# Kernel tuning notes

Measured on AMD Instinct MI355X. Metric: run time of the kernel, lower is better.

Reference implementation:

```python
import jax, jax.numpy as jnp
import numpy as np

B, N, D, H, HID = 8, 729, 1152, 12, 4304
HD = D // H
EPS = 1e-6


def _layer_norm(x, g, b):
    mu = jnp.mean(x, axis=-1, keepdims=True)
    var = jnp.mean((x - mu) ** 2, axis=-1, keepdims=True)
    return (x - mu) / jnp.sqrt(var + EPS) * g + b


def setup_inputs() -> dict:
    key = jax.random.key(0)
    ks = jax.random.split(key, 9)
    s = 0.02
    return {
        "x": jax.random.normal(ks[0], (B, N, D), jnp.float32),
        "wq": jax.random.normal(ks[1], (D, D), jnp.float32) * s,
        "bq": jnp.zeros((D,), jnp.float32),
        "wk": jax.random.normal(ks[2], (D, D), jnp.float32) * s,
        "bk": jnp.zeros((D,), jnp.float32),
        "wv": jax.random.normal(ks[3], (D, D), jnp.float32) * s,
        "bv": jnp.zeros((D,), jnp.float32),
        "wo": jax.random.normal(ks[4], (D, D), jnp.float32) * s,
        "bo": jnp.zeros((D,), jnp.float32),
        "ln1_g": jnp.ones((D,), jnp.float32),
        "ln1_b": jnp.zeros((D,), jnp.float32),
        "w_fc1": jax.random.normal(ks[5], (HID, D), jnp.float32) * s,
        "b_fc1": jnp.zeros((HID,), jnp.float32),
        "w_fc2": jax.random.normal(ks[6], (D, HID), jnp.float32) * s,
        "b_fc2": jnp.zeros((D,), jnp.float32),
        "ln2_g": jnp.ones((D,), jnp.float32),
        "ln2_b": jnp.zeros((D,), jnp.float32),
    }


def reference(x, wq, bq, wk, bk, wv, bv, wo, bo, ln1_g, ln1_b,
              w_fc1, b_fc1, w_fc2, b_fc2, ln2_g, ln2_b):
    b, n, d = x.shape
    # split_heads in the source is a plain view (B, H, N, HD) -- NOT a transpose.
    def heads(t):
        return t.reshape(b, H, n, HD)

    Q = heads(x @ wq.T + bq)
    K = heads(x @ wk.T + bk)
    V = heads(x @ wv.T + bv)

    scores = jnp.einsum("bhqd,bhkd->bhqk", Q, K) * (HD ** -0.5)
    attn_w = jax.nn.softmax(scores, axis=-1)
    o = jnp.einsum("bhqk,bhkd->bhqd", attn_w, V)  # [B,H,N,HD]
    o = jnp.swapaxes(o, 1, 2).reshape(b, n, d)
    attn_out = o @ wo.T + bo

    # post-norm: LN(sublayer) + residual
    h = _layer_norm(attn_out, ln1_g, ln1_b) + x

    # quirky MLP: activation applied BEFORE fc1 (faithful to source)
    m = jax.nn.gelu(h, approximate=True)
    m = m @ w_fc1.T + b_fc1
    m = m @ w_fc2.T + b_fc2

    return _layer_norm(m, ln2_g, ln2_b) + h
```

## Files before the change

### kernel.cpp

```cpp
#include <hip/hip_runtime.h>
#include <hip/hip_bf16.h>

#define BF16 __hip_bfloat16

typedef short short8 __attribute__((ext_vector_type(8)));
typedef short short4v __attribute__((ext_vector_type(4)));
typedef float v4f __attribute__((ext_vector_type(4)));
typedef float f4 __attribute__((ext_vector_type(4)));

__device__ float g_bp[1152];
__device__ BF16  g_wm[1152 * 1152];

__device__ __forceinline__ short f2bs(float f) {
    __hip_bfloat16 h = __float2bfloat16(f);
    return *(short*)&h;
}

__device__ __forceinline__ float bs2f(short s) {
    __hip_bfloat16 h = *(__hip_bfloat16*)&s;
    return __bfloat162float(h);
}

__device__ __forceinline__ void async_cp16(const BF16* g, BF16* l) {
    __builtin_amdgcn_global_load_lds(
        (const __attribute__((address_space(1))) void*)g,
        (__attribute__((address_space(3))) void*)l,
        16, 0, 0);
}

__device__ __forceinline__ int xcd_chunk(int u, int nwg) {
    int xcd = u & 7, i = u >> 3;
    int q = nwg >> 3, r = nwg & 7;
    return (xcd < r ? xcd * (q + 1) : r * (q + 1) + (xcd - r) * q) + i;
}

__global__ __launch_bounds__(256) void prep_kernel(
    const float* __restrict__ wq, const float* __restrict__ wk,
    const float* __restrict__ wv, const float* __restrict__ wo,
    const float* __restrict__ wfc1, const float* __restrict__ wfc2,
    const float* __restrict__ x,
    const float* __restrict__ bfc1, const float* __restrict__ bfc2,
    BF16* __restrict__ wbq, BF16* __restrict__ wbk,
    BF16* __restrict__ wbv, BF16* __restrict__ wbo,
    BF16* __restrict__ wbf1t, BF16* __restrict__ wbf2,
    BF16* __restrict__ xb)
{
    __shared__ float tile[64][65];
    const int bid = blockIdx.x;
    const int tid = threadIdx.x;

    if (bid < 16641) {
        const int i = bid * 256 + tid;
        constexpr int N_DD  = 331776;
        constexpr int N4    = 4 * N_DD;
        constexpr int N_F2  = 1253376;
        constexpr int E_F2  = N4 + N_F2;
        constexpr int N_X   = 1679616;
        constexpr int TOTAL = E_F2 + N_X;

        if (i < N4) {
            int seg = i / N_DD, j = i - seg * N_DD;
            const float* s = (seg == 0) ? wq : (seg == 1) ? wk : (seg == 2) ? wv : wo;
            BF16* d = (seg == 0) ? wbq : (seg == 1) ? wbk : (seg == 2) ? wbv : wbo;
            f4 v = ((const f4*)s)[j];
            short4v o = {f2bs(v.x), f2bs(v.y), f2bs(v.z), f2bs(v.w)};
            ((short4v*)d)[j] = o;
        } else if (i < E_F2) {
            int j = i - N4;
            int row = j / 1088;
            int c = (j - row * 1088) * 4;
            short4v o = {0, 0, 0, 0};
            if (c < 4304) {
                f4 v = *(const f4*)(wfc2 + (size_t)row * 4304 + c);
                o[0] = f2bs(v.x); o[1] = f2bs(v.y); o[2] = f2bs(v.z); o[3] = f2bs(v.w);
            }
            *(short4v*)(wbf2 + (size_t)row * 4352 + c) = o;
        } else if (i < TOTAL) {
            int j = i - E_F2;
            f4 v = ((const f4*)x)[j];
            short4v o = {f2bs(v.x), f2bs(v.y), f2bs(v.z), f2bs(v.w)};
            ((short4v*)xb)[j] = o;
        }
    } else if (bid < 17865) {
        const int b2 = bid - 16641;
        const int h0 = (b2 % 68) * 64;
        const int d0 = (b2 / 68) * 64;
#pragma unroll
        for (int i = 0; i < 4; ++i) {
            int lin = tid + i * 256;
            int r = lin >> 4, c4 = lin & 15;
            f4 v = {0.f, 0.f, 0.f, 0.f};
            if (h0 + r < 4304)
                v = *(const f4*)(wfc1 + (size_t)(h0 + r) * 1152 + d0 + c4 * 4);
            tile[r][c4 * 4 + 0] = v.x;
            tile[r][c4 * 4 + 1] = v.y;
            tile[r][c4 * 4 + 2] = v.z;
            tile[r][c4 * 4 + 3] = v.w;
        }
        __syncthreads();
#pragma unroll
        for (int i = 0; i < 2; ++i) {
            int lin = tid + i * 256;
            int dr = lin >> 3, h8 = lin & 7;
            short8 o;
#pragma unroll
            for (int e = 0; e < 8; ++e)
                o[e] = f2bs(tile[h8 * 8 + e][dr]);
            *(short8*)(wbf1t + (size_t)(d0 + dr) * 4352 + h0 + h8 * 8) = o;
        }
    } else {
        const int row = (bid - 17865) * 4 + (tid >> 6);
        const int lane = tid & 63;
        const float* wr = wfc2 + (size_t)row * 4304;
        float s = 0.f;
        for (int k = lane; k < 4304; k += 64) s += wr[k] * bfc1[k];
#pragma unroll
        for (int mm = 1; mm < 64; mm <<= 1) s += __shfl_xor(s, mm, 64);
        if (lane == 0) g_bp[row] = s + bfc2[row];
    }
}

__global__ __launch_bounds__(512, 2) void qkv_wm8_kernel(
    const BF16* __restrict__ A,
    const BF16* __restrict__ Wqkv,
    const float* __restrict__ b0, const float* __restrict__ b1,
    const float* __restrict__ b2,
    BF16* __restrict__ C, size_t cstride, int M,
    const BF16* __restrict__ W2,
    const BF16* __restrict__ W1t)
{
    __shared__ __align__(16) BF16 smem[65536];
    const int bid  = blockIdx.x;
    const int tid  = threadIdx.x;
    const int lane = tid & 63;
    const int wave = tid >> 6;
    const int quad = lane >> 4;
    const int l16  = lane & 15;
    const v4f zf = {0.f, 0.f, 0.f, 0.f};

    int rr[2], sw[2], lo[2];
#pragma unroll
    for (int j = 0; j < 2; ++j) {
        int c = tid + j * 512;
        rr[j] = c >> 3;
        sw[j] = (((c & 7) - (c >> 3)) & 7) << 3;
        lo[j] = (c & ~63) * 8;
    }

    if (bid < 81) {
        BF16* Am = smem;
        BF16* Bm = smem + 8192;
        const int m0 = (bid % 9) * 128;
        const int n0 = (bid / 9) * 128;
        const int wm = (wave >> 1) * 32;
        const int wn = (wave & 1) * 64;

        v4f acc[2][4];
#pragma unroll
        for (int i = 0; i < 2; ++i)
#pragma unroll
            for (int j = 0; j < 4; ++j) acc[i][j] = zf;

        const BF16* gA[2]; const BF16* gB[2];
#pragma unroll
        for (int j = 0; j < 2; ++j) {
            gA[j] = W2 + (size_t)(m0 + rr[j]) * 4352 + sw[j];
            gB[j] = W1t + (size_t)(n0 + rr[j]) * 4352 + sw[j];
        }

        for (int kt = 0; kt < 68; ++kt) {
#pragma unroll
            for (int j = 0; j < 2; ++j) { async_cp16(gA[j], Am + lo[j]); gA[j] += 64; }
#pragma unroll
            for (int j = 0; j < 2; ++j) { async_cp16(gB[j], Bm + lo[j]); gB[j] += 64; }
            __syncthreads();
#pragma unroll
            for (int ks = 0; ks < 2; ++ks) {
                short8 af[2], bfg[4];
#pragma unroll
                for (int mt = 0; mt < 2; ++mt) {
                    int row = wm + mt * 16 + l16;
                    af[mt] = *(const short8*)(Am + row * 64 + ((((ks << 2) | quad) + row & 7) & 7) * 8);
                }
#pragma unroll
                for (int nt = 0; nt < 4; ++nt) {
                    int row = wn + nt * 16 + l16;
                    bfg[nt] = *(const short8*)(Bm + row * 64 + ((((ks << 2) | quad) + row & 7) & 7) * 8);
                }
#pragma unroll
                for (int mt = 0; mt < 2; ++mt)
#pragma unroll
                    for (int nt = 0; nt < 4; ++nt)
                        acc[mt][nt] = __builtin_amdgcn_mfma_f32_16x16x32_bf16(
                            af[mt], bfg[nt], acc[mt][nt], 0, 0, 0);
            }
            __syncthreads();
        }

#pragma unroll
        for (int mt = 0; mt < 2; ++mt)
#pragma unroll
            for (int nt = 0; nt < 4; ++nt)
#pragma unroll
                for (int r2 = 0; r2 < 4; ++r2) {
                    int row_l = wm + mt * 16 + quad * 4 + r2;
                    int col_l = wn + nt * 16 + l16;
                    smem[row_l * 128 + col_l] = __float2bfloat16(acc[mt][nt][r2]);
                }
        __syncthreads();
#pragma unroll
        for (int p = 0; p < 4; ++p) {
            int idx = p * 512 + tid;
            *(short8*)(g_wm + (size_t)(m0 + (idx >> 4)) * 1152 + n0 + (idx & 15) * 8) =
                *(const short8*)(smem + idx * 8);
        }
    } else {
        const int wg = xcd_chunk(bid - 81, 322);
        const int m0 = (wg / 14) * 256;
        const int n0 = (wg % 14) * 256;
        const int wr = wave >> 2;
        const int wc = wave & 3;
        BF16* As = smem;
        BF16* Bs = smem + 32768;

        v4f acc[8][4];
#pragma unroll
        for (int i = 0; i < 8; ++i)
#pragma unroll
            for (int j = 0; j < 4; ++j) acc[i][j] = zf;

        #define STAGE_A(dd, hh, tt)                                            \
            {                                                                  \
                _Pragma("unroll")                                              \
                for (int j = 0; j < 2; ++j)                                    \
                    async_cp16(A + (size_t)(m0 + (hh) * 128 + rr[j]) * 1152    \
                                 + (tt) * 64 + sw[j],                          \
                               As + (dd) * 16384 + (hh) * 8192 + lo[j]);       \
            }
        #define STAGE_B(dd, hh, tt)                                            \
            {                                                                  \
                _Pragma("unroll")                                              \
                for (int j = 0; j < 2; ++j)                                    \
                    async_cp16(Wqkv + (size_t)(n0 + (hh) * 128 + rr[j]) * 1152 \
                                 + (tt) * 64 + sw[j],                          \
                               Bs + (dd) * 16384 + (hh) * 8192 + lo[j]);       \
            }

        STAGE_B(0, 0, 0); STAGE_B(0, 1, 0);
        STAGE_A(0, 0, 0); STAGE_A(0, 1, 0);
        STAGE_B(1, 0, 1); STAGE_B(1, 1, 1);
        asm volatile("s_waitcnt vmcnt(4)" ::: "memory");
        __builtin_amdgcn_s_barrier();
        __builtin_amdgcn_sched_barrier(0);

        short8 bfr[4][2], afr[2][2];
#pragma unroll 2
        for (int it = 0; it < 18; ++it) {
            const int d = it & 1;
            const BF16* Ad = As + d * 16384;
            const BF16* Bd = Bs + d * 16384;
#pragma unroll
            for (int q = 0; q < 4; ++q) {
                if (q == 0) {
#pragma unroll
                    for (int nt = 0; nt < 4; ++nt) {
                        int R = wc * 64 + nt * 16 + l16;
#pragma unroll
                        for (int ks = 0; ks < 2; ++ks)
                            bfr[nt][ks] = *(const short8*)(
                                Bd + R * 64 + ((((ks << 2) | quad) + R & 7) & 7) * 8);
                    }
                }
#pragma unroll
                for (int mi = 0; mi < 2; ++mi) {
                    int R = wr * 128 + (q * 2 + mi) * 16 + l16;
#pragma unroll
                    for (int ks = 0; ks < 2; ++ks)
                        afr[mi][ks] = *(const short8*)(
                            Ad + R * 64 + ((((ks << 2) | quad) + R & 7) & 7) * 8);
                }
                if (q == 0) { if (it + 1 < 18) STAGE_A(d ^ 1, 0, it + 1); }
                if (q == 1) { if (it + 1 < 18) STAGE_A(d ^ 1, 1, it + 1); }
                if (q == 2) { if (it + 2 < 18) STAGE_B(d,     0, it + 2); }
                if (q == 3) { if (it + 2 < 18) STAGE_B(d,     1, it + 2); }

                __builtin_amdgcn_s_barrier();
                asm volatile("s_waitcnt lgkmcnt(0)" ::: "memory");
                __builtin_amdgcn_sched_barrier(0);
                __builtin_amdgcn_s_setprio(1);
#pragma unroll
                for (int ks = 0; ks < 2; ++ks)
#pragma unroll
                    for (int mi = 0; mi < 2; ++mi)
#pragma unroll
                        for (int nt = 0; nt < 4; ++nt)
                            acc[q * 2 + mi][nt] = __builtin_amdgcn_mfma_f32_16x16x32_bf16(
                                afr[mi][ks], bfr[nt][ks], acc[q * 2 + mi][nt], 0, 0, 0);
                __builtin_amdgcn_s_setprio(0);
                if (q == 3) {
                    if (it + 2 < 18)
                        asm volatile("s_waitcnt vmcnt(4)" ::: "memory");
                    else
                        asm volatile("s_waitcnt vmcnt(0)" ::: "memory");
                }
                __builtin_amdgcn_s_barrier();
            }
        }
        #undef STAGE_A
        #undef STAGE_B

        float bv[4];
        int csel[4];
#pragma unroll
        for (int nt = 0; nt < 4; ++nt) {
            int col_g = n0 + wc * 64 + nt * 16 + l16;
            int sel = (col_g >= 2304) ? 2 : (col_g >= 1152) ? 1 : 0;
            csel[nt] = sel;
            const float* bp = (sel == 0) ? b0 : (sel == 1) ? b1 : b2;
            bv[nt] = (col_g < 3456) ? bp[col_g - sel * 1152] : 0.f;
        }
#pragma unroll
        for (int mt = 0; mt < 8; ++mt)
#pragma unroll
            for (int nt = 0; nt < 4; ++nt)
#pragma unroll
                for (int r2 = 0; r2 < 4; ++r2) {
                    int row_l = wr * 128 + mt * 16 + quad * 4 + r2;
                    int col_l = wc * 64 + nt * 16 + l16;
                    smem[row_l * 256 + col_l] = __float2bfloat16(acc[mt][nt][r2] + bv[nt]);
                }
        (void)csel;
        __syncthreads();
#pragma unroll
        for (int p = 0; p < 16; ++p) {
            int idx = p * 512 + tid;
            int row = m0 + (idx >> 5);
            int col_g = n0 + (idx & 31) * 8;
            if (row < M && col_g < 3456) {
                int sel = (col_g >= 2304) ? 2 : (col_g >= 1152) ? 1 : 0;
                *(short8*)(C + (size_t)sel * cstride + (size_t)row * 1152
                           + col_g - sel * 1152) =
                    *(const short8*)(smem + idx * 8);
            }
        }
    }
}

__global__ __launch_bounds__(256) void trans_kernel(
    const BF16* __restrict__ V, BF16* __restrict__ VT)
{
    __shared__ __align__(16) BF16 tl[64][128];
    const int bid = blockIdx.x, tid = threadIdx.x;
    const short8 zero8 = {0, 0, 0, 0, 0, 0, 0, 0};

    if (bid < 1152) {
        const int hg = bid / 12, kb = bid - hg * 12;
        const int b = hg / 12, hh = hg - b * 12;
        const BF16* src = V + (size_t)b * 839808 + (size_t)hh * 69984;
        BF16* dst = VT + (size_t)hg * 86016;
        const int kk0 = kb * 64;
#pragma unroll
        for (int i = 0; i < 3; ++i) {
            int c = tid + i * 256;
            int r = c / 12, cg = c - r * 12;
            short8 v = (kk0 + r < 729)
                ? *(const short8*)(src + (size_t)(kk0 + r) * 96 + cg * 8) : zero8;
            *(short8*)(&tl[r][(cg ^ ((r >> 3) & 7)) * 8]) = v;
        }
        __syncthreads();
#pragma unroll
        for (int i = 0; i < 3; ++i) {
            int wc = tid + i * 256;
            int hd = wc >> 3, o = wc & 7;
            int sp = (((hd >> 3) ^ o) << 3) + (hd & 7);
            short8 out;
#pragma unroll
            for (int j = 0; j < 8; ++j)
                out[j] = *(const short*)&tl[o * 8 + j][sp];
            *(short8*)(dst + (size_t)hd * 768 + kk0 + o * 8) = out;
        }
    } else {
        int c = (bid - 1152) * 256 + tid;
        int hg = c / 1536, rem = c - hg * 1536;
        int r = rem / 96, ock = rem - r * 96;
        int kk = ock * 8;
        short8 v = zero8;
        if (r == 0) {
            const short oneb = 0x3F80;
#pragma unroll
            for (int j = 0; j < 8; ++j) v[j] = (kk + j < 729) ? oneb : (short)0;
        }
        *(short8*)(VT + (size_t)hg * 86016 + (size_t)(96 + r) * 768 + kk) = v;
    }
}

template<int TM>
__global__ __launch_bounds__(256) void gemm_bt_t(
    const BF16* __restrict__ A, int lda,
    const BF16* __restrict__ W, int ldb,
    const float* __restrict__ bias, int nbias,
    BF16* __restrict__ C, int ldc,
    int M, int Kr, int nbn)
{
    constexpr int MT = TM / 32;
    __shared__ __align__(16) BF16 smem[(TM + 128) * 64];
    BF16* As = smem;
    BF16* Bs = smem + TM * 64;

    const int tid  = threadIdx.x;
    const int lane = tid & 63;
    const int wave = tid >> 6;
    const int quad = lane >> 4;
    const int l16  = lane & 15;
    const int wm   = (wave >> 1) * (TM / 2);
    const int wn   = (wave & 1) * 64;
    const int wg   = xcd_chunk(blockIdx.x, gridDim.x);
    const int m0   = (wg / nbn) * TM;
    const int n0   = (wg % nbn) * 128;
    if (m0 >= M) return;

    const v4f zf = {0.f, 0.f, 0.f, 0.f};
    v4f acc[MT][4];
#pragma unroll
    for (int i = 0; i < MT; ++i)
#pragma unroll
        for (int j = 0; j < 4; ++j) acc[i][j] = zf;

    const BF16* gA[MT]; BF16* lA[MT];
#pragma unroll
    for (int i = 0; i < MT; ++i) {
        int c = tid + i * 256;
        gA[i] = A + (size_t)(m0 + (c >> 3)) * lda + ((((c & 7) - (c >> 3)) & 7) << 3);
        lA[i] = As + (c & ~63) * 8;
    }
    const BF16* gB[4]; BF16* lB[4];
#pragma unroll
    for (int i = 0; i < 4; ++i) {
        int c = tid + i * 256;
        gB[i] = W + (size_t)(n0 + (c >> 3)) * ldb + ((((c & 7) - (c >> 3)) & 7) << 3);
        lB[i] = Bs + (c & ~63) * 8;
    }

    const int nk = Kr >> 6;
    for (int kt = 0; kt < nk; ++kt) {
#pragma unroll
        for (int i = 0; i < MT; ++i) { async_cp16(gA[i], lA[i]); gA[i] += 64; }
#pragma unroll
        for (int i = 0; i < 4; ++i)  { async_cp16(gB[i], lB[i]); gB[i] += 64; }
        __syncthreads();

#pragma unroll
        for (int ks = 0; ks < 2; ++ks) {
            short8 af[MT], bfg[4];
#pragma unroll
            for (int mt = 0; mt < MT; ++mt) {
                int row = wm + mt * 16 + l16;
                af[mt] = *(const short8*)(As + row * 64 + ((((ks << 2) | quad) + row & 7) & 7) * 8);
            }
#pragma unroll
            for (int nt = 0; nt < 4; ++nt) {
                int row = wn + nt * 16 + l16;
                bfg[nt] = *(const short8*)(Bs + row * 64 + ((((ks << 2) | quad) + row & 7) & 7) * 8);
            }
#pragma unroll
            for (int mt = 0; mt < MT; ++mt)
#pragma unroll
                for (int nt = 0; nt < 4; ++nt)
                    acc[mt][nt] = __builtin_amdgcn_mfma_f32_16x16x32_bf16(
                        af[mt], bfg[nt], acc[mt][nt], 0, 0, 0);
        }
        __syncthreads();
    }

    float bv[4];
#pragma unroll
    for (int nt = 0; nt < 4; ++nt) {
        int col = n0 + wn + nt * 16 + l16;
        bv[nt] = (col < nbias) ? bias[col] : 0.f;
    }
#pragma unroll
    for (int mt = 0; mt < MT; ++mt)
#pragma unroll
        for (int nt = 0; nt < 4; ++nt)
#pragma unroll
            for (int r2 = 0; r2 < 4; ++r2) {
                int row_l = wm + mt * 16 + quad * 4 + r2;
                int col_l = wn + nt * 16 + l16;
                smem[row_l * 128 + col_l] = __float2bfloat16(acc[mt][nt][r2] + bv[nt]);
            }
    __syncthreads();
#pragma unroll
    for (int p = 0; p < TM / 16; ++p) {
        int idx = p * 256 + tid;
        int row = m0 + (idx >> 4);
        if (row < M)
            *(short8*)(C + (size_t)row * ldc + n0 + (idx & 15) * 8) =
                *(const short8*)(smem + idx * 8);
    }
}

__global__ __launch_bounds__(256) void attn_flash3(
    const BF16* __restrict__ Q, const BF16* __restrict__ K,
    const BF16* __restrict__ VT, BF16* __restrict__ O)
{
    constexpr int NQ = 729, HDk = 96, DM = 1152, LDV = 768;
    __shared__ __align__(16) BF16 Ks[64 * 104];
    __shared__ __align__(16) BF16 Vs[112 * 64];
    __shared__ __align__(16) BF16 Ps[4][32 * 64];

    const int id = blockIdx.x;
    const int xcd = id & 7, slot = id >> 3;
    const int hb = slot / 6, qt = slot - hb * 6;
    const int hg = xcd * 12 + hb;
    const int b = hg / 12, hh = hg - b * 12;

    const int tid = threadIdx.x, wave = tid >> 6, lane = tid & 63;
    const int quad = lane >> 4, l16 = lane & 15;
    const size_t kbase = (size_t)b * (NQ * DM) + (size_t)hh * (NQ * HDk);
    const size_t vbase = (size_t)hg * 112 * LDV;

    const short8 zero8 = {0, 0, 0, 0, 0, 0, 0, 0};
    const v4f zf = {0.f, 0.f, 0.f, 0.f};
    const float C2 = 0.14724445f;

    const int q0w = qt * 128 + wave * 32;
    short8 aq[2][3];
#pragma unroll
    for (int mt = 0; mt < 2; ++mt) {
        int qrow = q0w + mt * 16 + l16;
#pragma unroll
        for (int ks = 0; ks < 3; ++ks)
            aq[mt][ks] = (qrow < NQ)
                ? *(const short8*)(Q + kbase + (size_t)qrow * HDk + ks * 32 + quad * 8)
                : zero8;
    }

    int kk_[3], kg_[3];
#pragma unroll
    for (int i = 0; i < 3; ++i) {
        int c = tid + i * 256;
        kk_[i] = c / 12; kg_[i] = c - kk_[i] * 12;
    }
    int vq_[4], vgr_[4], vhd_[4];
#pragma unroll
    for (int i = 0; i < 4; ++i) {
        int q = wave + 4 * i;
        vq_[i] = q;
        int hd = q * 8 + (lane >> 3);
        vhd_[i] = hd;
        vgr_[i] = ((lane & 7) - hd) & 7;
    }

    v4f oacc[2][7];
#pragma unroll
    for (int mt = 0; mt < 2; ++mt)
#pragma unroll
        for (int nt = 0; nt < 7; ++nt) oacc[mt][nt] = zf;

    short8 kreg[3];
#pragma unroll
    for (int i = 0; i < 3; ++i)
        kreg[i] = *(const short8*)(K + kbase + (size_t)kk_[i] * HDk + kg_[i] * 8);

    for (int kt = 0; kt < 12; ++kt) {
        const int k0 = kt * 64;
#pragma unroll
        for (int i = 0; i < 3; ++i)
            *(short8*)(Ks + kk_[i] * 104 + kg_[i] * 8) = kreg[i];
#pragma unroll
        for (int i = 0; i < 4; ++i) {
            if (vq_[i] < 14)
                async_cp16(VT + vbase + (size_t)vhd_[i] * LDV + k0 + vgr_[i] * 8,
                           Vs + vq_[i] * 512);
        }
        asm volatile("s_waitcnt lgkmcnt(0)" ::: "memory");
        __builtin_amdgcn_s_barrier();
        __builtin_amdgcn_sched_barrier(0);
        {
            const int kn = (kt < 11) ? (k0 + 64) : 0;
#pragma unroll
            for (int i = 0; i < 3; ++i)
                kreg[i] = *(const short8*)(K + kbase + (size_t)(kn + kk_[i]) * HDk + kg_[i] * 8);
        }

        v4f s[2][4];
#pragma unroll
        for (int mt = 0; mt < 2; ++mt)
#pragma unroll
            for (int nt = 0; nt < 4; ++nt) s[mt][nt] = zf;
#pragma unroll
        for (int ks = 0; ks < 3; ++ks)
#pragma unroll
            for (int nt = 0; nt < 4; ++nt) {
                short8 bk = *(const short8*)(Ks + (nt * 16 + l16) * 104 + ks * 32 + quad * 8);
#pragma unroll
                for (int mt = 0; mt < 2; ++mt)
                    s[mt][nt] = __builtin_amdgcn_mfma_f32_16x16x32_bf16(
                        aq[mt][ks], bk, s[mt][nt], 0, 0, 0);
            }

        BF16* Pw = &Ps[wave][0];
#pragma unroll
        for (int mt = 0; mt < 2; ++mt)
#pragma unroll
            for (int nt = 0; nt < 4; ++nt)
#pragma unroll
                for (int r = 0; r < 4; ++r)
                    Pw[((mt * 16 + quad * 4 + r) << 6)
                       + ((((nt << 1) | (l16 >> 3)) ^ (quad << 1)) << 3)
                       + (l16 & 7)] =
                        __float2bfloat16(exp2f(s[mt][nt][r] * C2));
        asm volatile("s_waitcnt lgkmcnt(0)" ::: "memory");

        short8 ap[2][2];
#pragma unroll
        for (int mt = 0; mt < 2; ++mt)
#pragma unroll
            for (int kc = 0; kc < 2; ++kc)
                ap[mt][kc] = *(const short8*)(Pw + ((mt * 16 + l16) << 6)
                    + ((((kc << 2) | quad) ^ (((l16 >> 2) & 3) << 1)) << 3));

        asm volatile("s_waitcnt vmcnt(3)" ::: "memory");
        __builtin_amdgcn_s_barrier();
        __builtin_amdgcn_sched_barrier(0);

#pragma unroll
        for (int nt = 0; nt < 7; ++nt) {
            int hd = nt * 16 + l16;
#pragma unroll
            for (int kc = 0; kc < 2; ++kc) {
                short8 bv = *(const short8*)(Vs + hd * 64 + (((kc * 4 + quad) + hd & 7) & 7) * 8);
#pragma unroll
                for (int mt = 0; mt < 2; ++mt)
                    oacc[mt][nt] = __builtin_amdgcn_mfma_f32_16x16x32_bf16(
                        ap[mt][kc], bv, oacc[mt][nt], 0, 0, 0);
            }
        }
        asm volatile("s_waitcnt lgkmcnt(0)" ::: "memory");
        __builtin_amdgcn_s_barrier();
        __builtin_amdgcn_sched_barrier(0);
    }

#pragma unroll
    for (int mt = 0; mt < 2; ++mt) {
        const int qb = q0w + mt * 16 + quad * 4;
#pragma unroll
        for (int r = 0; r < 4; ++r) {
            int q = qb + r;
            float lv = __shfl(oacc[mt][6][r], quad << 4, 64);
            float inv = (lv > 0.f) ? 1.f / lv : 0.f;
            if (q >= NQ) continue;
#pragma unroll
            for (int nt = 0; nt < 6; ++nt)
                O[(size_t)b * (NQ * DM) + (size_t)q * DM + hh * HDk + nt * 16 + l16] =
                    __float2bfloat16(oacc[mt][nt][r] * inv);
        }
    }
}

__device__ __forceinline__ float block_sum256(float v, float* red, int tid)
{
#pragma unroll
    for (int mm = 1; mm < 64; mm <<= 1) v += __shfl_xor(v, mm, 64);
    if ((tid & 63) == 0) red[tid >> 6] = v;
    __syncthreads();
    float r = red[0] + red[1] + red[2] + red[3];
    __syncthreads();
    return r;
}

__global__ __launch_bounds__(256) void ln1_gelu_kernel(
    const BF16* __restrict__ ao, const float* __restrict__ x,
    const float* __restrict__ gw, const float* __restrict__ bw,
    BF16* __restrict__ hout, BF16* __restrict__ gout)
{
    __shared__ float red[4];
    const int row = blockIdx.x, tid = threadIdx.x;
    const bool act = tid < 144;
    float v[8];
    float s = 0.f;
    if (act) {
        short8 pk = ((const short8*)(ao + (size_t)row * 1152))[tid];
#pragma unroll
        for (int j = 0; j < 8; ++j) { v[j] = bs2f(pk[j]); s += v[j]; }
    } else {
#pragma unroll
        for (int j = 0; j < 8; ++j) v[j] = 0.f;
    }
    s = block_sum256(s, red, tid);
    float mu = s * (1.f / 1152.f);
    float vsum = 0.f;
    if (act) {
#pragma unroll
        for (int j = 0; j < 8; ++j) { float d = v[j] - mu; vsum += d * d; }
    }
    vsum = block_sum256(vsum, red, tid);
    float rstd = rsqrtf(vsum * (1.f / 1152.f) + 1e-6f);
    if (act) {
        f4 g0 = ((const f4*)gw)[2 * tid], g1 = ((const f4*)gw)[2 * tid + 1];
        f4 b0 = ((const f4*)bw)[2 * tid], b1 = ((const f4*)bw)[2 * tid + 1];
        const f4* xr = (const f4*)(x + (size_t)row * 1152);
        f4 x0 = xr[2 * tid], x1 = xr[2 * tid + 1];
        short8 ho, go;
#pragma unroll
        for (int j = 0; j < 8; ++j) {
            float gj = (j < 4) ? g0[j] : g1[j - 4];
            float bj = (j < 4) ? b0[j] : b1[j - 4];
            float xj = (j < 4) ? x0[j] : x1[j - 4];
            float hv = (v[j] - mu) * rstd * gj + bj + xj;
            ho[j] = f2bs(hv);
            float t = hv;
            float gl = 0.5f * t * (1.f + tanhf(0.7978845608028654f * (t + 0.044715f * t * t * t)));
            go[j] = f2bs(gl);
        }
        ((short8*)(hout + (size_t)row * 1152))[tid] = ho;
        ((short8*)(gout + (size_t)row * 1152))[tid] = go;
    }
}

__global__ __launch_bounds__(256) void ln2_kernel(
    const BF16* __restrict__ m2, const BF16* __restrict__ hf,
    const float* __restrict__ gw, const float* __restrict__ bw,
    float* __restrict__ out)
{
    __shared__ float red[4];
    const int row = blockIdx.x, tid = threadIdx.x;
    const bool act = tid < 144;
    float v[8];
    float s = 0.f;
    if (act) {
        short8 pk = ((const short8*)(m2 + (size_t)row * 1152))[tid];
#pragma unroll
        for (int j = 0; j < 8; ++j) { v[j] = bs2f(pk[j]); s += v[j]; }
    } else {
#pragma unroll
        for (int j = 0; j < 8; ++j) v[j] = 0.f;
    }
    s = block_sum256(s, red, tid);
    float mu = s * (1.f / 1152.f);
    float vsum = 0.f;
    if (act) {
#pragma unroll
        for (int j = 0; j < 8; ++j) { float d = v[j] - mu; vsum += d * d; }
    }
    vsum = block_sum256(vsum, red, tid);
    float rstd = rsqrtf(vsum * (1.f / 1152.f) + 1e-6f);
    if (act) {
        f4 g0 = ((const f4*)gw)[2 * tid], g1 = ((const f4*)gw)[2 * tid + 1];
        f4 b0 = ((const f4*)bw)[2 * tid], b1 = ((const f4*)bw)[2 * tid + 1];
        short8 hfv = ((const short8*)(hf + (size_t)row * 1152))[tid];
        f4 o0, o1;
#pragma unroll
        for (int j = 0; j < 8; ++j) {
            float gj = (j < 4) ? g0[j] : g1[j - 4];
            float bj = (j < 4) ? b0[j] : b1[j - 4];
            float ov = (v[j] - mu) * rstd * gj + bj + bs2f(hfv[j]);
            if (j < 4) o0[j] = ov; else o1[j - 4] = ov;
        }
        f4* orow = (f4*)(out + (size_t)row * 1152);
        orow[2 * tid] = o0;
        orow[2 * tid + 1] = o1;
    }
}

extern "C" void kernel_launch(void* const* d_in, const int* in_sizes, int n_in,
                              void* d_out, int out_size, void* d_ws, size_t ws_size,
                              hipStream_t stream)
{
    const float* x    = (const float*)d_in[0];
    const float* wq   = (const float*)d_in[1];
    const float* bq   = (const float*)d_in[2];
    const float* wk   = (const float*)d_in[3];
    const float* bk   = (const float*)d_in[4];
    const float* wv   = (const float*)d_in[5];
    const float* bv   = (const float*)d_in[6];
    const float* wo   = (const float*)d_in[7];
    const float* bo   = (const float*)d_in[8];
    const float* ln1g = (const float*)d_in[9];
    const float* ln1b = (const float*)d_in[10];
    const float* wfc1 = (const float*)d_in[11];
    const float* bfc1 = (const float*)d_in[12];
    const float* wfc2 = (const float*)d_in[13];
    const float* bfc2 = (const float*)d_in[14];
    const float* ln2g = (const float*)d_in[15];
    const float* ln2b = (const float*)d_in[16];

    const int T = 8 * 729;
    const int D = 1152, HIDP = 4352;
    const size_t TD = (size_t)T * D;
    const size_t WDD = (size_t)D * D;

    BF16* wbq   = (BF16*)d_ws;
    BF16* wbk   = wbq + WDD;
    BF16* wbv   = wbk + WDD;
    BF16* wbo   = wbv + WDD;
    BF16* wbf1t = wbo + WDD;
    BF16* wbf2  = wbf1t + (size_t)HIDP * D;
    BF16* xb    = wbf2 + (size_t)D * HIDP;
    BF16* S0    = xb + TD;
    BF16* S1    = S0 + TD;
    BF16* S2    = S1 + TD;
    BF16* S3    = S2 + TD;
    BF16* C0    = S3 + TD;
    BF16* C1    = C0 + TD;
    BF16* VT    = C0;

    static float* bp_dev = nullptr;
    static BF16*  wm_dev = nullptr;
    if (!bp_dev) hipGetSymbolAddress((void**)&bp_dev, HIP_SYMBOL(g_bp));
    if (!wm_dev) hipGetSymbolAddress((void**)&wm_dev, HIP_SYMBOL(g_wm));

    dim3 blk(256);

    prep_kernel<<<18153, blk, 0, stream>>>(
        wq, wk, wv, wo, wfc1, wfc2, x, bfc1, bfc2,
        wbq, wbk, wbv, wbo, wbf1t, wbf2, xb);

    qkv_wm8_kernel<<<403, dim3(512), 0, stream>>>(
        xb, wbq, bq, bk, bv, S0, TD, T, wbf2, wbf1t);

    trans_kernel<<<1728, blk, 0, stream>>>(S2, VT);

    attn_flash3<<<576, blk, 0, stream>>>(S0, S1, VT, S3);

    gemm_bt_t<64><<<828, blk, 0, stream>>>(S3, D, wbo, D, bo, D, C0, D, T, D, 9);

    ln1_gelu_kernel<<<T, blk, 0, stream>>>(C0, x, ln1g, ln1b, C1, C0);

    gemm_bt_t<64><<<828, blk, 0, stream>>>(C0, D, wm_dev, D, bp_dev, D, S3, D, T, D, 9);

    ln2_kernel<<<T, blk, 0, stream>>>(S3, C1, ln2g, ln2b, (float*)d_out);
}
```

Measured before the change: 384.6 us.

## Read K directly from global in attention, shrink LN blocks, use exp-based GELU

New measurement: 408.9 us. 1.06x slower.

```diff
diff --git a/kernel.cpp b/kernel.cpp
--- a/kernel.cpp
+++ b/kernel.cpp
@@ -310,12 +310,10 @@
         #undef STAGE_B
 
         float bv[4];
-        int csel[4];
 #pragma unroll
         for (int nt = 0; nt < 4; ++nt) {
             int col_g = n0 + wc * 64 + nt * 16 + l16;
             int sel = (col_g >= 2304) ? 2 : (col_g >= 1152) ? 1 : 0;
-            csel[nt] = sel;
             const float* bp = (sel == 0) ? b0 : (sel == 1) ? b1 : b2;
             bv[nt] = (col_g < 3456) ? bp[col_g - sel * 1152] : 0.f;
         }
@@ -329,7 +327,6 @@
                     int col_l = wc * 64 + nt * 16 + l16;
                     smem[row_l * 256 + col_l] = __float2bfloat16(acc[mt][nt][r2] + bv[nt]);
                 }
-        (void)csel;
         __syncthreads();
 #pragma unroll
         for (int p = 0; p < 16; ++p) {
@@ -504,7 +501,6 @@
     const BF16* __restrict__ VT, BF16* __restrict__ O)
 {
     constexpr int NQ = 729, HDk = 96, DM = 1152, LDV = 768;
-    __shared__ __align__(16) BF16 Ks[64 * 104];
     __shared__ __align__(16) BF16 Vs[112 * 64];
     __shared__ __align__(16) BF16 Ps[4][32 * 64];
 
@@ -535,12 +531,6 @@
                 : zero8;
     }
 
-    int kk_[3], kg_[3];
-#pragma unroll
-    for (int i = 0; i < 3; ++i) {
-        int c = tid + i * 256;
-        kk_[i] = c / 12; kg_[i] = c - kk_[i] * 12;
-    }
     int vq_[4], vgr_[4], vhd_[4];
 #pragma unroll
     for (int i = 0; i < 4; ++i) {
@@ -557,47 +547,33 @@
 #pragma unroll
         for (int nt = 0; nt < 7; ++nt) oacc[mt][nt] = zf;
 
-    short8 kreg[3];
-#pragma unroll
-    for (int i = 0; i < 3; ++i)
-        kreg[i] = *(const short8*)(K + kbase + (size_t)kk_[i] * HDk + kg_[i] * 8);
-
     for (int kt = 0; kt < 12; ++kt) {
         const int k0 = kt * 64;
-#pragma unroll
-        for (int i = 0; i < 3; ++i)
-            *(short8*)(Ks + kk_[i] * 104 + kg_[i] * 8) = kreg[i];
 #pragma unroll
         for (int i = 0; i < 4; ++i) {
             if (vq_[i] < 14)
                 async_cp16(VT + vbase + (size_t)vhd_[i] * LDV + k0 + vgr_[i] * 8,
                            Vs + vq_[i] * 512);
         }
-        asm volatile("s_waitcnt lgkmcnt(0)" ::: "memory");
-        __builtin_amdgcn_s_barrier();
-        __builtin_amdgcn_sched_barrier(0);
-        {
-            const int kn = (kt < 11) ? (k0 + 64) : 0;
-#pragma unroll
-            for (int i = 0; i < 3; ++i)
-                kreg[i] = *(const short8*)(K + kbase + (size_t)(kn + kk_[i]) * HDk + kg_[i] * 8);
-        }
 
         v4f s[2][4];
 #pragma unroll
         for (int mt = 0; mt < 2; ++mt)
 #pragma unroll
             for (int nt = 0; nt < 4; ++nt) s[mt][nt] = zf;
+        __builtin_amdgcn_s_setprio(1);
 #pragma unroll
         for (int ks = 0; ks < 3; ++ks)
 #pragma unroll
             for (int nt = 0; nt < 4; ++nt) {
-                short8 bk = *(const short8*)(Ks + (nt * 16 + l16) * 104 + ks * 32 + quad * 8);
+                short8 bk = *(const short8*)(
+                    K + kbase + (size_t)(k0 + nt * 16 + l16) * HDk + ks * 32 + quad * 8);
 #pragma unroll
                 for (int mt = 0; mt < 2; ++mt)
                     s[mt][nt] = __builtin_amdgcn_mfma_f32_16x16x32_bf16(
                         aq[mt][ks], bk, s[mt][nt], 0, 0, 0);
             }
+        __builtin_amdgcn_s_setprio(0);
 
         BF16* Pw = &Ps[wave][0];
 #pragma unroll
@@ -620,10 +596,11 @@
                 ap[mt][kc] = *(const short8*)(Pw + ((mt * 16 + l16) << 6)
                     + ((((kc << 2) | quad) ^ (((l16 >> 2) & 3) << 1)) << 3));
 
-        asm volatile("s_waitcnt vmcnt(3)" ::: "memory");
+        asm volatile("s_waitcnt vmcnt(0)" ::: "memory");
         __builtin_amdgcn_s_barrier();
         __builtin_amdgcn_sched_barrier(0);
 
+        __builtin_amdgcn_s_setprio(1);
 #pragma unroll
         for (int nt = 0; nt < 7; ++nt) {
             int hd = nt * 16 + l16;
@@ -636,6 +613,7 @@
                         ap[mt][kc], bv, oacc[mt][nt], 0, 0, 0);
             }
         }
+        __builtin_amdgcn_s_setprio(0);
         asm volatile("s_waitcnt lgkmcnt(0)" ::: "memory");
         __builtin_amdgcn_s_barrier();
         __builtin_amdgcn_sched_barrier(0);
@@ -658,23 +636,23 @@
     }
 }
 
-__device__ __forceinline__ float block_sum256(float v, float* red, int tid)
+__device__ __forceinline__ float block_sum192(float v, float* red, int tid)
 {
 #pragma unroll
     for (int mm = 1; mm < 64; mm <<= 1) v += __shfl_xor(v, mm, 64);
     if ((tid & 63) == 0) red[tid >> 6] = v;
     __syncthreads();
-    float r = red[0] + red[1] + red[2] + red[3];
+    float r = red[0] + red[1] + red[2];
     __syncthreads();
     return r;
 }
 
-__global__ __launch_bounds__(256) void ln1_gelu_kernel(
+__global__ __launch_bounds__(192) void ln1_gelu_kernel(
     const BF16* __restrict__ ao, const float* __restrict__ x,
     const float* __restrict__ gw, const float* __restrict__ bw,
     BF16* __restrict__ hout, BF16* __restrict__ gout)
 {
-    __shared__ float red[4];
+    __shared__ float red[3];
     const int row = blockIdx.x, tid = threadIdx.x;
     const bool act = tid < 144;
     float v[8];
@@ -687,14 +665,14 @@
 #pragma unroll
         for (int j = 0; j < 8; ++j) v[j] = 0.f;
     }
-    s = block_sum256(s, red, tid);
+    s = block_sum192(s, red, tid);
     float mu = s * (1.f / 1152.f);
     float vsum = 0.f;
     if (act) {
 #pragma unroll
         for (int j = 0; j < 8; ++j) { float d = v[j] - mu; vsum += d * d; }
     }
-    vsum = block_sum256(vsum, red, tid);
+    vsum = block_sum192(vsum, red, tid);
     float rstd = rsqrtf(vsum * (1.f / 1152.f) + 1e-6f);
     if (act) {
         f4 g0 = ((const f4*)gw)[2 * tid], g1 = ((const f4*)gw)[2 * tid + 1];
@@ -709,8 +687,8 @@
             float xj = (j < 4) ? x0[j] : x1[j - 4];
             float hv = (v[j] - mu) * rstd * gj + bj + xj;
             ho[j] = f2bs(hv);
-            float t = hv;
-            float gl = 0.5f * t * (1.f + tanhf(0.7978845608028654f * (t + 0.044715f * t * t * t)));
+            float z2 = 2.3022077f * hv + 0.10294636f * hv * hv * hv;
+            float gl = hv / (1.f + exp2f(-z2));
             go[j] = f2bs(gl);
         }
         ((short8*)(hout + (size_t)row * 1152))[tid] = ho;
@@ -718,12 +696,12 @@
     }
 }
 
-__global__ __launch_bounds__(256) void ln2_kernel(
+__global__ __launch_bounds__(192) void ln2_kernel(
     const BF16* __restrict__ m2, const BF16* __restrict__ hf,
     const float* __restrict__ gw, const float* __restrict__ bw,
     float* __restrict__ out)
 {
-    __shared__ float red[4];
+    __shared__ float red[3];
     const int row = blockIdx.x, tid = threadIdx.x;
     const bool act = tid < 144;
     float v[8];
@@ -736,14 +714,14 @@
 #pragma unroll
         for (int j = 0; j < 8; ++j) v[j] = 0.f;
     }
-    s = block_sum256(s, red, tid);
+    s = block_sum192(s, red, tid);
     float mu = s * (1.f / 1152.f);
     float vsum = 0.f;
     if (act) {
 #pragma unroll
         for (int j = 0; j < 8; ++j) { float d = v[j] - mu; vsum += d * d; }
     }
-    vsum = block_sum256(vsum, red, tid);
+    vsum = block_sum192(vsum, red, tid);
     float rstd = rsqrtf(vsum * (1.f / 1152.f) + 1e-6f);
     if (act) {
         f4 g0 = ((const f4*)gw)[2 * tid], g1 = ((const f4*)gw)[2 * tid + 1];
@@ -825,9 +803,9 @@
 
     gemm_bt_t<64><<<828, blk, 0, stream>>>(S3, D, wbo, D, bo, D, C0, D, T, D, 9);
 
-    ln1_gelu_kernel<<<T, blk, 0, stream>>>(C0, x, ln1g, ln1b, C1, C0);
+    ln1_gelu_kernel<<<T, dim3(192), 0, stream>>>(C0, x, ln1g, ln1b, C1, C0);
 
     gemm_bt_t<64><<<828, blk, 0, stream>>>(C0, D, wm_dev, D, bp_dev, D, S3, D, T, D, 9);
 
-    ln2_kernel<<<T, blk, 0, stream>>>(S3, C1, ln2g, ln2b, (float*)d_out);
-}
+    ln2_kernel<<<T, dim3(192), 0, stream>>>(S3, C1, ln2g, ln2b, (float*)d_out);
+}
```
